# Performance work log

Hardware: AMD Instinct MI355X
Metric: run time of the kernel (lower is better)

The kernel has to match this reference:

```python
import jax, jax.numpy as jnp
import numpy as np

N = 100000      # nodes
E = 1600000     # edges
G = 256         # graphs
NF = 2          # dataset.num_features
NC = 2          # dataset.num_classes
DIM = 32
BN_EPS = 1e-5


def _gin_layer(h, src, dst, w_in, b_in, w_out, b_out, gamma, beta):
    # GINConv (eps=0): h' = MLP(h + sum_{j in N(i)} h_j)
    agg = jax.ops.segment_sum(h[src], dst, num_segments=N)  # [N, d] scatter-add
    z = h + agg
    z = jax.nn.relu(z @ w_in + b_in) @ w_out + b_out        # 2-layer MLP
    z = jax.nn.relu(z)
    # BatchNorm1d (training-mode batch stats, biased var as in torch)
    mean = jnp.mean(z, axis=0)
    var = jnp.var(z, axis=0)
    return gamma * (z - mean) * jax.lax.rsqrt(var + BN_EPS) + beta


def setup_inputs() -> dict:
    key = jax.random.key(0)
    ks = jax.random.split(key, 20)
    s = 0.1
    x = jax.random.normal(ks[0], (N, NF), dtype=jnp.float32)
    edge_index = jax.random.randint(ks[1], (2, E), 0, N, dtype=jnp.int64)
    batch = jnp.sort(jax.random.randint(ks[2], (N,), 0, G, dtype=jnp.int64))
    return {
        "x": x,
        "edge_index": edge_index,
        "batch": batch,
        "w1_in": jax.random.normal(ks[3], (NF, DIM), dtype=jnp.float32) * s,
        "b1_in": jnp.zeros((DIM,), jnp.float32),
        "w1_out": jax.random.normal(ks[4], (DIM, DIM), dtype=jnp.float32) * s,
        "b1_out": jnp.zeros((DIM,), jnp.float32),
        "ws_in": jax.random.normal(ks[5], (4, DIM, DIM), dtype=jnp.float32) * s,
        "bs_in": jnp.zeros((4, DIM), jnp.float32),
        "ws_out": jax.random.normal(ks[6], (4, DIM, DIM), dtype=jnp.float32) * s,
        "bs_out": jnp.zeros((4, DIM), jnp.float32),
        "bn_gamma": jnp.ones((5, DIM), jnp.float32),
        "bn_beta": jnp.zeros((5, DIM), jnp.float32),
        "fc1_w": jax.random.normal(ks[7], (DIM, DIM), dtype=jnp.float32) * s,
        "fc1_b": jnp.zeros((DIM,), jnp.float32),
        "fc2_w": jax.random.normal(ks[8], (DIM, NC), dtype=jnp.float32) * s,
        "fc2_b": jnp.zeros((NC,), jnp.float32),
    }


def reference(x, edge_index, batch, w1_in, b1_in, w1_out, b1_out,
              ws_in, bs_in, ws_out, bs_out, bn_gamma, bn_beta,
              fc1_w, fc1_b, fc2_w, fc2_b):
    src, dst = edge_index[0], edge_index[1]
    h = _gin_layer(x, src, dst, w1_in, b1_in, w1_out, b1_out, bn_gamma[0], bn_beta[0])
    for i in range(4):  # convs 2..5 (structurally identical)
        h = _gin_layer(h, src, dst, ws_in[i], bs_in[i], ws_out[i], bs_out[i],
                       bn_gamma[i + 1], bn_beta[i + 1])
    g = jax.ops.segment_sum(h, batch, num_segments=G)  # global_add_pool -> [G, DIM]
    g = jax.nn.relu(g @ fc1_w + fc1_b)
    # dropout is identity in eval mode
    g = g @ fc2_w + fc2_b
    return jax.nn.log_softmax(g, axis=-1)
```

## Files before the change

kernel.cpp:

```cpp
#include <hip/hip_runtime.h>
#include <math.h>

#define NN 100000
#define NE 1600000
#define NG 256
#define NPART 200
#define PS 500
#define CAP 9000
#define EPB 2048
#define NBLK ((NE + EPB - 1) / EPB)
#define DEGB 64
static constexpr float BN_EPS = 1e-5f;

__device__ inline float h2f(unsigned short u) {
    _Float16 h; __builtin_memcpy(&h, &u, 2); return (float)h;
}
__device__ inline unsigned short f2h(float f) {
    _Float16 h = (_Float16)f; unsigned short u; __builtin_memcpy(&u, &h, 2); return u;
}
__device__ inline unsigned int pack2(float a, float b) {
    return (unsigned int)f2h(a) | ((unsigned int)f2h(b) << 16);
}

__global__ __launch_bounds__(256) void bucket_k(const int* __restrict__ src,
                                                const int* __restrict__ dst,
                                                int* __restrict__ bcur,
                                                unsigned int* __restrict__ bpk) {
    __shared__ int cnt[NPART];
    __shared__ int base[NPART];
    int t = threadIdx.x;
    for (int i = t; i < NPART; i += 256) cnt[i] = 0;
    __syncthreads();
    int eb = blockIdx.x * EPB + t * 8;
    bool act = eb < NE;
    int myp[8], myr[8];
    unsigned int pk[8];
    if (act) {
        int4 d0 = *reinterpret_cast<const int4*>(dst + eb);
        int4 d1 = *reinterpret_cast<const int4*>(dst + eb + 4);
        int4 s0 = *reinterpret_cast<const int4*>(src + eb);
        int4 s1 = *reinterpret_cast<const int4*>(src + eb + 4);
        int dd[8] = {d0.x,d0.y,d0.z,d0.w,d1.x,d1.y,d1.z,d1.w};
        int ss[8] = {s0.x,s0.y,s0.z,s0.w,s1.x,s1.y,s1.z,s1.w};
        #pragma unroll
        for (int i = 0; i < 8; i++) {
            int p = dd[i] / PS;
            myp[i] = p;
            pk[i] = ((unsigned int)ss[i] << 9) | (unsigned int)(dd[i] - p * PS);
            myr[i] = atomicAdd(&cnt[p], 1);
        }
    }
    __syncthreads();
    for (int i = t; i < NPART; i += 256)
        base[i] = cnt[i] ? atomicAdd(&bcur[i], cnt[i]) : 0;
    __syncthreads();
    if (act) {
        #pragma unroll
        for (int i = 0; i < 8; i++)
            bpk[myp[i] * CAP + base[myp[i]] + myr[i]] = pk[i];
    }
}

__global__ __launch_bounds__(256) void build_k(const int* __restrict__ bcur,
                                               const unsigned int* __restrict__ bpk,
                                               int* __restrict__ rowptr,
                                               int* __restrict__ csr,
                                               int* __restrict__ perm) {
    __shared__ int hist[PS];
    __shared__ int allc[NPART];
    __shared__ int psum[256];
    __shared__ int bc[DEGB];
    int p = blockIdx.x, t = threadIdx.x;
    int lo = p * PS;
    if (t < NPART) allc[t] = bcur[t];
    for (int i = t; i < PS; i += 256) hist[i] = 0;
    if (t < DEGB) bc[t] = 0;
    __syncthreads();
    int base = 0;
    for (int q = 0; q < p; q++) base += allc[q];
    int cnt = allc[p];
    const unsigned int* bp = bpk + p * CAP;
    const uint4* bp4 = reinterpret_cast<const uint4*>(bp);
    int n4 = cnt >> 2;
    for (int i = t; i < n4; i += 256) {
        uint4 v = bp4[i];
        atomicAdd(&hist[v.x & 511u], 1);
        atomicAdd(&hist[v.y & 511u], 1);
        atomicAdd(&hist[v.z & 511u], 1);
        atomicAdd(&hist[v.w & 511u], 1);
    }
    for (int i = 4 * n4 + t; i < cnt; i += 256) atomicAdd(&hist[bp[i] & 511u], 1);
    __syncthreads();
    int j0 = t * 2;
    int d0v = 0, d1v = 0, tsum = 0;
    if (j0 < PS) {
        d0v = hist[j0]; d1v = hist[j0 + 1];
        tsum = d0v + d1v;
        atomicAdd(&bc[d0v < DEGB ? d0v : DEGB - 1], 1);
        atomicAdd(&bc[d1v < DEGB ? d1v : DEGB - 1], 1);
    }
    psum[t] = tsum;
    __syncthreads();
    for (int off = 1; off < 256; off <<= 1) {
        int v = (t >= off) ? psum[t - off] : 0;
        __syncthreads();
        psum[t] += v;
        __syncthreads();
    }
    int texcl = psum[t] - tsum;
    if (j0 < PS) {
        int run = base + texcl;
        hist[j0] = run; rowptr[lo + j0] = run; run += d0v;
        hist[j0 + 1] = run; rowptr[lo + j0 + 1] = run; run += d1v;
    }
    if (p == NPART - 1 && t == 0) rowptr[NN] = base + cnt;
    __syncthreads();
    if (t == 0) {
        int run = 0;
        #pragma unroll
        for (int b = 0; b < DEGB; b++) { int c = bc[b]; bc[b] = run; run += c; }
    }
    __syncthreads();
    if (j0 < PS) {
        int r0 = atomicAdd(&bc[d0v < DEGB ? d0v : DEGB - 1], 1);
        perm[lo + r0] = lo + j0;
        int r1 = atomicAdd(&bc[d1v < DEGB ? d1v : DEGB - 1], 1);
        perm[lo + r1] = lo + j0 + 1;
    }
    __syncthreads();
    for (int i = t; i < n4; i += 256) {
        uint4 v = bp4[i];
        csr[atomicAdd(&hist[v.x & 511u], 1)] = v.x >> 9;
        csr[atomicAdd(&hist[v.y & 511u], 1)] = v.y >> 9;
        csr[atomicAdd(&hist[v.z & 511u], 1)] = v.z >> 9;
        csr[atomicAdd(&hist[v.w & 511u], 1)] = v.w >> 9;
    }
    for (int i = 4 * n4 + t; i < cnt; i += 256)
        csr[atomicAdd(&hist[bp[i] & 511u], 1)] = bp[i] >> 9;
}

__global__ __launch_bounds__(64) void gmlp1_k(
        const float* __restrict__ x, const int* __restrict__ perm,
        const int* __restrict__ rowptr, const int* __restrict__ csr,
        const float* __restrict__ w_in, const float* __restrict__ b_in,
        const float* __restrict__ w_out, const float* __restrict__ b_out,
        unsigned short* __restrict__ zout, float* __restrict__ stats) {
    __shared__ float lwi[64], lbi[32], lwo[1024], lbo[32];
    __shared__ float zl[64][33];
    int t = threadIdx.x;
    lwi[t] = w_in[t];
    if (t < 32) { lbi[t] = b_in[t]; lbo[t] = b_out[t]; }
    for (int i = t; i < 1024; i += 64) lwo[i] = w_out[i];
    __syncthreads();
    int gid = blockIdx.x * 64 + t;
    if (gid < NN) {
        int node = perm[gid];
        float2 self = *reinterpret_cast<const float2*>(x + 2 * (size_t)node);
        float h0 = self.x, h1 = self.y;
        float g0 = 0.f, g1 = 0.f;
        int rs = rowptr[node], re = rowptr[node + 1];
        int k = rs;
        for (; k + 4 <= re; k += 4) {
            int s0 = csr[k], s1 = csr[k+1], s2 = csr[k+2], s3 = csr[k+3];
            float2 v0 = *reinterpret_cast<const float2*>(x + 2 * (size_t)s0);
            float2 v1 = *reinterpret_cast<const float2*>(x + 2 * (size_t)s1);
            float2 v2 = *reinterpret_cast<const float2*>(x + 2 * (size_t)s2);
            float2 v3 = *reinterpret_cast<const float2*>(x + 2 * (size_t)s3);
            h0 += v0.x + v2.x; h1 += v0.y + v2.y;
            g0 += v1.x + v3.x; g1 += v1.y + v3.y;
        }
        for (; k < re; k++) {
            int s = csr[k];
            float2 v = *reinterpret_cast<const float2*>(x + 2 * (size_t)s);
            h0 += v.x; h1 += v.y;
        }
        h0 += g0; h1 += g1;
        float y[32];
        #pragma unroll
        for (int kk = 0; kk < 32; kk++) {
            float a = lbi[kk] + h0 * lwi[kk] + h1 * lwi[32 + kk];
            y[kk] = a > 0.f ? a : 0.f;
        }
        float z[32];
        #pragma unroll 4
        for (int kk = 0; kk < 32; kk++) {
            float a = lbo[kk];
            #pragma unroll
            for (int c = 0; c < 32; c++) a += y[c] * lwo[c * 32 + kk];
            z[kk] = a > 0.f ? a : 0.f;
        }
        uint4* zo = reinterpret_cast<uint4*>(zout + (size_t)node * 32);
        #pragma unroll
        for (int kk = 0; kk < 4; kk++) {
            uint4 w;
            w.x = pack2(z[8*kk+0], z[8*kk+1]);
            w.y = pack2(z[8*kk+2], z[8*kk+3]);
            w.z = pack2(z[8*kk+4], z[8*kk+5]);
            w.w = pack2(z[8*kk+6], z[8*kk+7]);
            zo[kk] = w;
        }
        #pragma unroll
        for (int kk = 0; kk < 32; kk++) zl[t][kk] = z[kk];
    } else {
        for (int kk = 0; kk < 32; kk++) zl[t][kk] = 0.f;
    }
    __syncthreads();
    if (t < 32) {
        float s = 0.f, sq = 0.f;
        for (int n = 0; n < 64; n++) { float v = zl[n][t]; s += v; sq += v * v; }
        atomicAdd(&stats[t], s);
        atomicAdd(&stats[32 + t], sq);
    }
}

__global__ __launch_bounds__(256) void gmlp32_k(
        const unsigned short* __restrict__ z, const int* __restrict__ perm,
        const float* __restrict__ statsIn,
        const float* __restrict__ gamma, const float* __restrict__ beta,
        const int* __restrict__ rowptr, const int* __restrict__ csr,
        const float* __restrict__ w_in, const float* __restrict__ b_in,
        const float* __restrict__ w_out, const float* __restrict__ b_out,
        unsigned short* __restrict__ zout, float* __restrict__ statsOut) {
    __shared__ float lwi[1024], lwo[1024], lbi[32], lbo[32], lsc[64];
    __shared__ float zin[128][33];
    int t = threadIdx.x;
    int n = t >> 1, q = t & 1, c0 = q * 16;
    for (int i = t; i < 1024; i += 256) { lwi[i] = w_in[i]; lwo[i] = w_out[i]; }
    if (t < 32) {
        lbi[t] = b_in[t]; lbo[t] = b_out[t];
        float mean = statsIn[t] * (1.f / NN);
        float var  = statsIn[32 + t] * (1.f / NN) - mean * mean;
        float scale = gamma[t] * rsqrtf(var + BN_EPS);
        lsc[t] = scale;
        lsc[32 + t] = beta[t] - mean * scale;
    }
    __syncthreads();
    int gid = blockIdx.x * 128 + n;
    bool act = gid < NN;
    int node = act ? perm[gid] : 0;
    float a[16];
    #pragma unroll
    for (int j = 0; j < 16; j++) a[j] = 0.f;
    float cntf = 0.f;
    if (act) {
        int rs = rowptr[node], re = rowptr[node + 1];
        cntf = (float)(re - rs + 1);
        const unsigned short* zb = z + (size_t)node * 32 + c0;
        uint4 sa = *reinterpret_cast<const uint4*>(zb);
        uint4 sb = *reinterpret_cast<const uint4*>(zb + 8);
        const unsigned short* pa = reinterpret_cast<const unsigned short*>(&sa);
        const unsigned short* pb = reinterpret_cast<const unsigned short*>(&sb);
        #pragma unroll
        for (int j = 0; j < 8; j++) { a[j] = h2f(pa[j]); a[8 + j] = h2f(pb[j]); }
        int k = rs;
        for (; k + 4 <= re; k += 4) {
            int s0 = csr[k], s1 = csr[k + 1], s2 = csr[k + 2], s3 = csr[k + 3];
            const unsigned short* r0 = z + (size_t)s0 * 32 + c0;
            const unsigned short* r1 = z + (size_t)s1 * 32 + c0;
            const unsigned short* r2 = z + (size_t)s2 * 32 + c0;
            const unsigned short* r3 = z + (size_t)s3 * 32 + c0;
            uint4 v0a = *reinterpret_cast<const uint4*>(r0);
            uint4 v0b = *reinterpret_cast<const uint4*>(r0 + 8);
            uint4 v1a = *reinterpret_cast<const uint4*>(r1);
            uint4 v1b = *reinterpret_cast<const uint4*>(r1 + 8);
            uint4 v2a = *reinterpret_cast<const uint4*>(r2);
            uint4 v2b = *reinterpret_cast<const uint4*>(r2 + 8);
            uint4 v3a = *reinterpret_cast<const uint4*>(r3);
            uint4 v3b = *reinterpret_cast<const uint4*>(r3 + 8);
            const unsigned short* q0a = reinterpret_cast<const unsigned short*>(&v0a);
            const unsigned short* q0b = reinterpret_cast<const unsigned short*>(&v0b);
            const unsigned short* q1a = reinterpret_cast<const unsigned short*>(&v1a);
            const unsigned short* q1b = reinterpret_cast<const unsigned short*>(&v1b);
            const unsigned short* q2a = reinterpret_cast<const unsigned short*>(&v2a);
            const unsigned short* q2b = reinterpret_cast<const unsigned short*>(&v2b);
            const unsigned short* q3a = reinterpret_cast<const unsigned short*>(&v3a);
            const unsigned short* q3b = reinterpret_cast<const unsigned short*>(&v3b);
            #pragma unroll
            for (int j = 0; j < 8; j++) {
                a[j]     += (h2f(q0a[j]) + h2f(q1a[j])) + (h2f(q2a[j]) + h2f(q3a[j]));
                a[8 + j] += (h2f(q0b[j]) + h2f(q1b[j])) + (h2f(q2b[j]) + h2f(q3b[j]));
            }
        }
        for (; k < re; k++) {
            int s = csr[k];
            const unsigned short* r = z + (size_t)s * 32 + c0;
            uint4 va = *reinterpret_cast<const uint4*>(r);
            uint4 vb = *reinterpret_cast<const uint4*>(r + 8);
            const unsigned short* qa = reinterpret_cast<const unsigned short*>(&va);
            const unsigned short* qb = reinterpret_cast<const unsigned short*>(&vb);
            #pragma unroll
            for (int j = 0; j < 8; j++) { a[j] += h2f(qa[j]); a[8 + j] += h2f(qb[j]); }
        }
    }
    #pragma unroll
    for (int j = 0; j < 16; j++)
        zin[n][c0 + j] = act ? (a[j] * lsc[c0 + j] + cntf * lsc[32 + c0 + j]) : 0.f;
    __syncthreads();
    float y[16];
    #pragma unroll
    for (int j = 0; j < 16; j++) y[j] = lbi[c0 + j];
    #pragma unroll
    for (int c = 0; c < 32; c++) {
        float zv = zin[n][c];
        #pragma unroll
        for (int j = 0; j < 16; j++) y[j] += zv * lwi[c * 32 + c0 + j];
    }
    #pragma unroll
    for (int j = 0; j < 16; j++) y[j] = y[j] > 0.f ? y[j] : 0.f;
    __syncthreads();
    #pragma unroll
    for (int j = 0; j < 16; j++) zin[n][c0 + j] = y[j];
    __syncthreads();
    float o[16];
    #pragma unroll
    for (int j = 0; j < 16; j++) o[j] = lbo[c0 + j];
    #pragma unroll
    for (int c = 0; c < 32; c++) {
        float yv = zin[n][c];
        #pragma unroll
        for (int j = 0; j < 16; j++) o[j] += yv * lwo[c * 32 + c0 + j];
    }
    #pragma unroll
    for (int j = 0; j < 16; j++) o[j] = o[j] > 0.f ? o[j] : 0.f;
    if (act) {
        unsigned short* zo = zout + (size_t)node * 32 + c0;
        uint4 wa, wb;
        wa.x = pack2(o[0], o[1]);   wa.y = pack2(o[2], o[3]);
        wa.z = pack2(o[4], o[5]);   wa.w = pack2(o[6], o[7]);
        wb.x = pack2(o[8], o[9]);   wb.y = pack2(o[10], o[11]);
        wb.z = pack2(o[12], o[13]); wb.w = pack2(o[14], o[15]);
        *reinterpret_cast<uint4*>(zo) = wa;
        *reinterpret_cast<uint4*>(zo + 8) = wb;
    }
    __syncthreads();
    #pragma unroll
    for (int j = 0; j < 16; j++) zin[n][c0 + j] = act ? o[j] : 0.f;
    __syncthreads();
    if (t < 32) {
        float s = 0.f, sq = 0.f;
        for (int nn = 0; nn < 128; nn++) {
            float v = zin[nn][t];
            s += v; sq += v * v;
        }
        atomicAdd(&statsOut[t], s);
        atomicAdd(&statsOut[32 + t], sq);
    }
}

__global__ __launch_bounds__(256) void pool_seg_k(
        const unsigned short* __restrict__ z,
        const float* __restrict__ statsIn,
        const float* __restrict__ gamma, const float* __restrict__ beta,
        const int* __restrict__ batch, float* __restrict__ g) {
    __shared__ float lsc[64];
    __shared__ float part[32][33];
    int t = threadIdx.x, slot = t >> 3, q = t & 7, c0 = q * 4;
    int gr = blockIdx.x;
    if (t < 32) {
        float mean = statsIn[t] * (1.f / NN);
        float var  = statsIn[32 + t] * (1.f / NN) - mean * mean;
        float scale = gamma[t] * rsqrtf(var + BN_EPS);
        lsc[t] = scale;
        lsc[32 + t] = beta[t] - mean * scale;
    }
    int lo = 0, hi = NN;
    while (lo < hi) { int mid = (lo + hi) >> 1; if (batch[mid] < gr) lo = mid + 1; else hi = mid; }
    int start = lo;
    hi = NN;
    while (lo < hi) { int mid = (lo + hi) >> 1; if (batch[mid] < gr + 1) lo = mid + 1; else hi = mid; }
    int end = lo;
    float a0 = 0.f, a1 = 0.f, a2 = 0.f, a3 = 0.f;
    for (int i = start + slot; i < end; i += 32) {
        ushort4 v = *reinterpret_cast<const ushort4*>(z + (size_t)i * 32 + c0);
        a0 += h2f(v.x); a1 += h2f(v.y); a2 += h2f(v.z); a3 += h2f(v.w);
    }
    part[slot][c0+0] = a0; part[slot][c0+1] = a1;
    part[slot][c0+2] = a2; part[slot][c0+3] = a3;
    __syncthreads();
    if (t < 32) {
        float s = 0.f;
        for (int sl = 0; sl < 32; sl++) s += part[sl][t];
        float cnt = (float)(end - start);
        g[(size_t)gr * 32 + t] = s * lsc[t] + cnt * lsc[32 + t];
    }
}

__global__ __launch_bounds__(256) void head_k(
        const float* __restrict__ g,
        const float* __restrict__ fc1w, const float* __restrict__ fc1b,
        const float* __restrict__ fc2w, const float* __restrict__ fc2b,
        float* __restrict__ out) {
    __shared__ float lw1[1024], lb1[32], lw2[64], lb2[2];
    int t = threadIdx.x;
    for (int i = t; i < 1024; i += 256) lw1[i] = fc1w[i];
    if (t < 32) lb1[t] = fc1b[t];
    if (t < 64) lw2[t] = fc2w[t];
    if (t < 2) lb2[t] = fc2b[t];
    __syncthreads();
    float gv[32];
    #pragma unroll
    for (int c = 0; c < 32; c++) gv[c] = g[(size_t)t * 32 + c];
    float o0 = lb2[0], o1 = lb2[1];
    #pragma unroll 4
    for (int k = 0; k < 32; k++) {
        float a = lb1[k];
        #pragma unroll
        for (int c = 0; c < 32; c++) a += gv[c] * lw1[c * 32 + k];
        a = a > 0.f ? a : 0.f;
        o0 += a * lw2[k * 2 + 0];
        o1 += a * lw2[k * 2 + 1];
    }
    float m = fmaxf(o0, o1);
    float lse = m + logf(expf(o0 - m) + expf(o1 - m));
    out[t * 2 + 0] = o0 - lse;
    out[t * 2 + 1] = o1 - lse;
}

extern "C" void kernel_launch(void* const* d_in, const int* in_sizes, int n_in,
                              void* d_out, int out_size, void* d_ws, size_t ws_size,
                              hipStream_t stream) {
    const float* x      = (const float*)d_in[0];
    const int*   ei     = (const int*)d_in[1];
    const int*   src    = ei;
    const int*   dst    = ei + NE;
    const int*   batch  = (const int*)d_in[2];
    const float* w1_in  = (const float*)d_in[3];
    const float* b1_in  = (const float*)d_in[4];
    const float* w1_out = (const float*)d_in[5];
    const float* b1_out = (const float*)d_in[6];
    const float* ws_in  = (const float*)d_in[7];
    const float* bs_in  = (const float*)d_in[8];
    const float* ws_out = (const float*)d_in[9];
    const float* bs_out = (const float*)d_in[10];
    const float* gamma  = (const float*)d_in[11];
    const float* beta   = (const float*)d_in[12];
    const float* fc1w   = (const float*)d_in[13];
    const float* fc1b   = (const float*)d_in[14];
    const float* fc2w   = (const float*)d_in[15];
    const float* fc2b   = (const float*)d_in[16];
    float* out = (float*)d_out;

    unsigned short* bufA = (unsigned short*)d_ws;
    unsigned short* bufB = bufA + (size_t)NN * 32;
    float* stats  = (float*)(bufB + (size_t)NN * 32);
    int*   bcur   = (int*)(stats + 5 * 64);
    float* g      = (float*)(bcur + NPART);
    int*   perm   = (int*)(g + (size_t)NG * 32);
    int*   rowptr = perm + NN;
    int*   csr    = rowptr + NN + 4;
    unsigned int* bpk = (unsigned int*)(csr + NE);

    hipMemsetAsync(stats, 0, (size_t)(5 * 64 + NPART) * sizeof(int), stream);

    bucket_k<<<NBLK, 256, 0, stream>>>(src, dst, bcur, bpk);
    build_k<<<NPART, 256, 0, stream>>>(bcur, bpk, rowptr, csr, perm);

    gmlp1_k<<<(NN + 63) / 64, 64, 0, stream>>>(x, perm, rowptr, csr,
                                               w1_in, b1_in, w1_out, b1_out, bufA, stats);

    const unsigned short* cur = bufA;
    unsigned short* nxt = bufB;
    for (int j = 0; j < 4; j++) {
        gmlp32_k<<<(NN + 127) / 128, 256, 0, stream>>>(cur, perm, stats + j * 64,
                                              gamma + j * 32, beta + j * 32,
                                              rowptr, csr,
                                              ws_in + j * 1024, bs_in + j * 32,
                                              ws_out + j * 1024, bs_out + j * 32,
                                              nxt, stats + (j + 1) * 64);
        unsigned short* tmp = (unsigned short*)cur; cur = nxt; nxt = tmp;
    }

    pool_seg_k<<<NG, 256, 0, stream>>>(cur, stats + 4 * 64,
                                       gamma + 4 * 32, beta + 4 * 32, batch, g);
    head_k<<<1, 256, 0, stream>>>(g, fc1w, fc1b, fc2w, fc2b, out);
}
```

Baseline: 413.3 us.

## Split first GIN layer work across two threads per node

The first-layer kernel now uses 256-thread blocks covering 128 nodes, with two threads per node. Each thread gathers alternating neighbours and the partial sums are combined with a lane shuffle. Each thread then computes half of the 32 MLP outputs, with the hidden activations shared through LDS. This aims to cut per-thread register pressure and serial work in the first layer, and it mirrors the layout already used by the 32-wide layers. The cost is extra block barriers and an LDS round trip.

Result: faster. 389.4 us (-5.8%).

```diff
diff --git a/kernel.cpp b/kernel.cpp
--- a/kernel.cpp
+++ b/kernel.cpp
@@ -139,29 +139,34 @@
         csr[atomicAdd(&hist[bp[i] & 511u], 1)] = bp[i] >> 9;
 }
 
-__global__ __launch_bounds__(64) void gmlp1_k(
+__global__ __launch_bounds__(256) void gmlp1_k(
         const float* __restrict__ x, const int* __restrict__ perm,
         const int* __restrict__ rowptr, const int* __restrict__ csr,
         const float* __restrict__ w_in, const float* __restrict__ b_in,
         const float* __restrict__ w_out, const float* __restrict__ b_out,
         unsigned short* __restrict__ zout, float* __restrict__ stats) {
     __shared__ float lwi[64], lbi[32], lwo[1024], lbo[32];
-    __shared__ float zl[64][33];
+    __shared__ float zin[128][33];
     int t = threadIdx.x;
-    lwi[t] = w_in[t];
+    int n = t >> 1, q = t & 1, c0 = q * 16;
+    for (int i = t; i < 1024; i += 256) lwo[i] = w_out[i];
+    if (t < 64) lwi[t] = w_in[t];
     if (t < 32) { lbi[t] = b_in[t]; lbo[t] = b_out[t]; }
-    for (int i = t; i < 1024; i += 64) lwo[i] = w_out[i];
-    __syncthreads();
-    int gid = blockIdx.x * 64 + t;
-    if (gid < NN) {
-        int node = perm[gid];
-        float2 self = *reinterpret_cast<const float2*>(x + 2 * (size_t)node);
-        float h0 = self.x, h1 = self.y;
+    __syncthreads();
+    int gid = blockIdx.x * 128 + n;
+    bool act = gid < NN;
+    int node = act ? perm[gid] : 0;
+    float h0 = 0.f, h1 = 0.f;
+    if (act) {
+        int rs = rowptr[node], re = rowptr[node + 1];
+        if (q == 0) {
+            float2 self = *reinterpret_cast<const float2*>(x + 2 * (size_t)node);
+            h0 = self.x; h1 = self.y;
+        }
         float g0 = 0.f, g1 = 0.f;
-        int rs = rowptr[node], re = rowptr[node + 1];
-        int k = rs;
-        for (; k + 4 <= re; k += 4) {
-            int s0 = csr[k], s1 = csr[k+1], s2 = csr[k+2], s3 = csr[k+3];
+        int k = rs + q;
+        for (; k + 6 < re; k += 8) {
+            int s0 = csr[k], s1 = csr[k + 2], s2 = csr[k + 4], s3 = csr[k + 6];
             float2 v0 = *reinterpret_cast<const float2*>(x + 2 * (size_t)s0);
             float2 v1 = *reinterpret_cast<const float2*>(x + 2 * (size_t)s1);
             float2 v2 = *reinterpret_cast<const float2*>(x + 2 * (size_t)s2);
@@ -169,45 +174,55 @@
             h0 += v0.x + v2.x; h1 += v0.y + v2.y;
             g0 += v1.x + v3.x; g1 += v1.y + v3.y;
         }
-        for (; k < re; k++) {
+        for (; k < re; k += 2) {
             int s = csr[k];
             float2 v = *reinterpret_cast<const float2*>(x + 2 * (size_t)s);
             h0 += v.x; h1 += v.y;
         }
         h0 += g0; h1 += g1;
-        float y[32];
-        #pragma unroll
-        for (int kk = 0; kk < 32; kk++) {
-            float a = lbi[kk] + h0 * lwi[kk] + h1 * lwi[32 + kk];
-            y[kk] = a > 0.f ? a : 0.f;
-        }
-        float z[32];
-        #pragma unroll 4
-        for (int kk = 0; kk < 32; kk++) {
-            float a = lbo[kk];
-            #pragma unroll
-            for (int c = 0; c < 32; c++) a += y[c] * lwo[c * 32 + kk];
-            z[kk] = a > 0.f ? a : 0.f;
-        }
-        uint4* zo = reinterpret_cast<uint4*>(zout + (size_t)node * 32);
-        #pragma unroll
-        for (int kk = 0; kk < 4; kk++) {
-            uint4 w;
-            w.x = pack2(z[8*kk+0], z[8*kk+1]);
-            w.y = pack2(z[8*kk+2], z[8*kk+3]);
-            w.z = pack2(z[8*kk+4], z[8*kk+5]);
-            w.w = pack2(z[8*kk+6], z[8*kk+7]);
-            zo[kk] = w;
-        }
-        #pragma unroll
-        for (int kk = 0; kk < 32; kk++) zl[t][kk] = z[kk];
-    } else {
-        for (int kk = 0; kk < 32; kk++) zl[t][kk] = 0.f;
-    }
+    }
+    h0 += __shfl_xor(h0, 1);
+    h1 += __shfl_xor(h1, 1);
+    float y[16];
+    #pragma unroll
+    for (int j = 0; j < 16; j++) {
+        float a = lbi[c0 + j] + h0 * lwi[c0 + j] + h1 * lwi[32 + c0 + j];
+        y[j] = a > 0.f ? a : 0.f;
+    }
+    #pragma unroll
+    for (int j = 0; j < 16; j++) zin[n][c0 + j] = act ? y[j] : 0.f;
+    __syncthreads();
+    float o[16];
+    #pragma unroll
+    for (int j = 0; j < 16; j++) o[j] = lbo[c0 + j];
+    #pragma unroll
+    for (int c = 0; c < 32; c++) {
+        float yv = zin[n][c];
+        #pragma unroll
+        for (int j = 0; j < 16; j++) o[j] += yv * lwo[c * 32 + c0 + j];
+    }
+    #pragma unroll
+    for (int j = 0; j < 16; j++) o[j] = o[j] > 0.f ? o[j] : 0.f;
+    if (act) {
+        unsigned short* zo = zout + (size_t)node * 32 + c0;
+        uint4 wa, wb;
+        wa.x = pack2(o[0], o[1]);   wa.y = pack2(o[2], o[3]);
+        wa.z = pack2(o[4], o[5]);   wa.w = pack2(o[6], o[7]);
+        wb.x = pack2(o[8], o[9]);   wb.y = pack2(o[10], o[11]);
+        wb.z = pack2(o[12], o[13]); wb.w = pack2(o[14], o[15]);
+        *reinterpret_cast<uint4*>(zo) = wa;
+        *reinterpret_cast<uint4*>(zo + 8) = wb;
+    }
+    __syncthreads();
+    #pragma unroll
+    for (int j = 0; j < 16; j++) zin[n][c0 + j] = act ? o[j] : 0.f;
     __syncthreads();
     if (t < 32) {
         float s = 0.f, sq = 0.f;
-        for (int n = 0; n < 64; n++) { float v = zl[n][t]; s += v; sq += v * v; }
+        for (int nn = 0; nn < 128; nn++) {
+            float v = zin[nn][t];
+            s += v; sq += v * v;
+        }
         atomicAdd(&stats[t], s);
         atomicAdd(&stats[32 + t], sq);
     }
@@ -455,8 +470,8 @@
     bucket_k<<<NBLK, 256, 0, stream>>>(src, dst, bcur, bpk);
     build_k<<<NPART, 256, 0, stream>>>(bcur, bpk, rowptr, csr, perm);
 
-    gmlp1_k<<<(NN + 63) / 64, 64, 0, stream>>>(x, perm, rowptr, csr,
-                                               w1_in, b1_in, w1_out, b1_out, bufA, stats);
+    gmlp1_k<<<(NN + 127) / 128, 256, 0, stream>>>(x, perm, rowptr, csr,
+                                                  w1_in, b1_in, w1_out, b1_out, bufA, stats);
 
     const unsigned short* cur = bufA;
     unsigned short* nxt = bufB;
```
